# Optimization experiments

Measured on AMD Instinct MI355X. Metric: run time of the kernel, lower is better.

Reference implementation:

```python
import jax, jax.numpy as jnp
import numpy as np

F = 32        # nFilters
OPS = 5       # numOfOps (len(ratio))
CIN = 32      # in_planes of each filter's conv
N, H, W = 16, 128, 128
EPS = 1e-5    # BatchNorm2d default eps
RATIO = [0.3125, 0.3125, 0.1875, 0.125, 0.0625]


def setup_inputs() -> dict:
    key = jax.random.key(0)
    k1, k2 = jax.random.split(key, 2)
    x = jax.random.normal(k1, (N, CIN, H, W), jnp.float32)
    # each filter holds OPS weight variants (one per quantization op); 1 output channel each
    W_all = jax.random.normal(k2, (F, OPS, CIN, 3, 3), jnp.float32) * 0.05
    gamma = jnp.ones((F,), jnp.float32)
    beta = jnp.zeros((F,), jnp.float32)
    # setFiltersRatio: assign op index i to int(ratio[i]*F) consecutive filters
    counts = [int(r * F) for r in RATIO]
    counts[-1] = F - sum(counts[:-1])
    op_idx = jnp.asarray(np.repeat(np.arange(OPS), counts), jnp.int32)  # [F]
    return {"x": x, "W_all": W_all, "gamma": gamma, "beta": beta, "op_idx": op_idx}


def reference(x, W_all, gamma, beta, op_idx):
    # per-filter selection of the active op's conv weight (irregular gather)
    Wsel = W_all[jnp.arange(W_all.shape[0]), op_idx]  # [F, CIN, 3, 3]
    # all per-filter 1-out-channel convs of the same x == one grouped conv to F channels
    out1 = jax.lax.conv_general_dilated(
        x, Wsel, window_strides=(1, 1), padding="SAME",
        dimension_numbers=("NCHW", "OIHW", "NCHW"))  # [N, F, H, W]
    # BatchNorm2d in training mode: batch statistics over (N, H, W) per channel
    mean = out1.mean(axis=(0, 2, 3), keepdims=True)
    var = ((out1 - mean) ** 2).mean(axis=(0, 2, 3), keepdims=True)
    out1 = (out1 - mean) * jax.lax.rsqrt(var + EPS)
    out1 = out1 * gamma[None, :, None, None] + beta[None, :, None, None]
    # op[1] per filter: (quantized) ReLU activation — same math for every op variant
    return jax.nn.relu(out1)
```

## Files before the change

### kernel.cpp

```cpp
#include <hip/hip_runtime.h>

#define NB   16
#define CINC 32
#define HH   128
#define WWD  128
#define FF   32
#define OPSN 5
#define EPSV 1e-5f

#define WS_PARTIAL_FOFF 64
#define WS_WFRAG_BOFF   262400
#define WS_XT_BOFF      280832
#define WS_NEED         (280832 + (size_t)16*130*130*32*2)

typedef __attribute__((ext_vector_type(8))) short bf16x8;
typedef __attribute__((ext_vector_type(4))) float f32x4;
typedef __attribute__((ext_vector_type(4))) unsigned int u32x4;

__device__ __forceinline__ unsigned short f2bf(float f) {
    unsigned u = __builtin_bit_cast(unsigned, f);
    u += 0x7FFFu + ((u >> 16) & 1u);
    return (unsigned short)(u >> 16);
}
__device__ __forceinline__ unsigned pack2(float lo, float hi) {
    return (unsigned)f2bf(lo) | ((unsigned)f2bf(hi) << 16);
}

__global__ __launch_bounds__(256) void transform_kernel(
    const float* __restrict__ x, const float* __restrict__ Wall,
    const int* __restrict__ opidx, unsigned short* __restrict__ xt,
    unsigned short* __restrict__ wfrag)
{
    __shared__ float lds[128 * 35];
    const int bid = blockIdx.x;
    const int tid = threadIdx.x;

    if (bid == NB * 130) {
        for (int idx = tid; idx < 9216; idx += 256) {
            int frag = idx >> 9;
            int lane = (idx >> 3) & 63;
            int j    = idx & 7;
            int s = frag >> 1, m = frag & 1;
            int kh = s / 3, kw = s - 3 * kh;
            int f = m * 16 + (lane & 15);
            int c = ((lane >> 4) << 3) + j;
            float v = Wall[((size_t)(f * OPSN + opidx[f]) * 288) + c * 9 + kh * 3 + kw];
            wfrag[idx] = f2bf(v);
        }
        return;
    }

    const int idx = bid >> 3;
    const int n   = (bid & 7) * 2 + (idx / 130);
    const int hp  = idx % 130;

    unsigned short* rowp = xt + (size_t)(n * 130 + hp) * 130 * 32;
    uint4 zz = make_uint4(0, 0, 0, 0);

    if (hp == 0 || hp == 129) {
        for (int c = tid; c < 520; c += 256) ((uint4*)rowp)[c] = zz;
        return;
    }

    const int h = hp - 1;
    const float* xr = x + ((size_t)n * CINC * HH + h) * WWD;
    const int c  = tid >> 3;
    const int wq = tid & 7;
#pragma unroll
    for (int it = 0; it < 4; ++it) {
        int w4 = wq + it * 8;
        f32x4 v = __builtin_nontemporal_load(
            (const f32x4*)(xr + (size_t)c * (HH * WWD)) + w4);
        int w = w4 * 4;
        lds[(w + 0) * 35 + c] = v.x;
        lds[(w + 1) * 35 + c] = v.y;
        lds[(w + 2) * 35 + c] = v.z;
        lds[(w + 3) * 35 + c] = v.w;
    }
    __syncthreads();
    for (int cc = tid; cc < 512; cc += 256) {
        int p = cc >> 2, k = cc & 3;
        const float* s = &lds[p * 35 + k * 8];
        uint4 o;
        o.x = pack2(s[0], s[1]); o.y = pack2(s[2], s[3]);
        o.z = pack2(s[4], s[5]); o.w = pack2(s[6], s[7]);
        ((uint4*)rowp)[4 + cc] = o;
    }
    if (tid < 4)       ((uint4*)rowp)[tid] = zz;
    else if (tid < 8)  ((uint4*)rowp)[129 * 4 + tid - 4] = zz;
}

#define LOADROW(f0, f1, f2, R)                                                  \
    {                                                                           \
        const unsigned short* rp =                                              \
            xbase + ((size_t)(R) * 130 + w0) * 32 + laneoff;                    \
        f0 = *(const bf16x8*)(rp);                                              \
        f1 = *(const bf16x8*)(rp + 32);                                         \
        f2 = *(const bf16x8*)(rp + 64);                                         \
    }

#define MROW(f0, f1, f2, aA, aB, kh)                                            \
    {                                                                           \
        aA = __builtin_amdgcn_mfma_f32_16x16x32_bf16(wfr[2*((kh)*3+0)],   f0, aA, 0,0,0); \
        aB = __builtin_amdgcn_mfma_f32_16x16x32_bf16(wfr[2*((kh)*3+0)+1], f0, aB, 0,0,0); \
        aA = __builtin_amdgcn_mfma_f32_16x16x32_bf16(wfr[2*((kh)*3+1)],   f1, aA, 0,0,0); \
        aB = __builtin_amdgcn_mfma_f32_16x16x32_bf16(wfr[2*((kh)*3+1)+1], f1, aB, 0,0,0); \
        aA = __builtin_amdgcn_mfma_f32_16x16x32_bf16(wfr[2*((kh)*3+2)],   f2, aA, 0,0,0); \
        aB = __builtin_amdgcn_mfma_f32_16x16x32_bf16(wfr[2*((kh)*3+2)+1], f2, aB, 0,0,0); \
    }

#define CONV_PROLOGUE                                                           \
    bf16x8 wfr[18];                                                             \
    _Pragma("unroll")                                                           \
    for (int i = 0; i < 18; ++i)                                                \
        wfr[i] = *(const bf16x8*)(wfrag + (i * 64 + lane) * 8);                 \
    const unsigned short* xbase = xt + (size_t)n * 130 * 130 * 32;              \
    const int laneoff = l15 * 32 + lhi * 8;                                     \
    f32x4 zz4 = {0.f, 0.f, 0.f, 0.f};                                           \
    f32x4 a0A = zz4, a0B = zz4, a1A = zz4, a1B = zz4;                           \
    f32x4 a2A = zz4, a2B = zz4, a3A = zz4, a3B = zz4;                           \
    bf16x8 c0, c1, c2, n0, n1, n2;                                              \
    LOADROW(c0, c1, c2, h0);                                                    \
    LOADROW(n0, n1, n2, h0 + 1);

#define CONV_BODY(FIN)                                                          \
    MROW(c0, c1, c2, a0A, a0B, 0);                                              \
    LOADROW(c0, c1, c2, h0 + 2);                                                \
    MROW(n0, n1, n2, a0A, a0B, 1);                                              \
    MROW(n0, n1, n2, a1A, a1B, 0);                                              \
    LOADROW(n0, n1, n2, h0 + 3);                                                \
    MROW(c0, c1, c2, a0A, a0B, 2);                                              \
    MROW(c0, c1, c2, a1A, a1B, 1);                                              \
    MROW(c0, c1, c2, a2A, a2B, 0);                                              \
    FIN(a0A, a0B, 0);                                                           \
    LOADROW(c0, c1, c2, h0 + 4);                                                \
    MROW(n0, n1, n2, a1A, a1B, 2);                                              \
    MROW(n0, n1, n2, a2A, a2B, 1);                                              \
    MROW(n0, n1, n2, a3A, a3B, 0);                                              \
    FIN(a1A, a1B, 1);                                                           \
    LOADROW(n0, n1, n2, h0 + 5);                                                \
    MROW(c0, c1, c2, a2A, a2B, 2);                                              \
    MROW(c0, c1, c2, a3A, a3B, 1);                                              \
    FIN(a2A, a2B, 2);                                                           \
    MROW(n0, n1, n2, a3A, a3B, 2);                                              \
    FIN(a3A, a3B, 3);

__global__ __launch_bounds__(256) void conv_stats_kernel(
    const unsigned short* __restrict__ xt,
    const unsigned short* __restrict__ wfrag,
    float* __restrict__ partial)
{
    __shared__ float red[4][64];
    const int bid  = blockIdx.x;
    const int tid  = threadIdx.x;
    const int n    = (bid & 7) * 2 + ((bid >> 3) & 1);
    const int rest = bid >> 4;
    const int h0   = (rest & 31) * 4;
    const int wh   = rest >> 5;
    const int lane = tid & 63;
    const int wv   = tid >> 6;
    const int w0   = wh * 64 + wv * 16;
    const int l15  = lane & 15, lhi = lane >> 4;

    float s8[8], q8[8];
#pragma unroll
    for (int j = 0; j < 8; ++j) { s8[j] = 0.f; q8[j] = 0.f; }

#define FIN_STATS(aA, aB, hh)                                                   \
    {                                                                           \
        _Pragma("unroll")                                                       \
        for (int r = 0; r < 4; ++r) {                                           \
            float v0 = aA[r], v1 = aB[r];                                       \
            s8[r]     += v0;  q8[r]     += v0 * v0;                             \
            s8[4 + r] += v1;  q8[4 + r] += v1 * v1;                             \
        }                                                                       \
    }

    CONV_PROLOGUE
    CONV_BODY(FIN_STATS)
#undef FIN_STATS

#pragma unroll
    for (int m = 1; m < 16; m <<= 1) {
#pragma unroll
        for (int j = 0; j < 8; ++j) {
            s8[j] += __shfl_xor(s8[j], m, 64);
            q8[j] += __shfl_xor(q8[j], m, 64);
        }
    }
    if (l15 == 0) {
#pragma unroll
        for (int j = 0; j < 8; ++j) {
            int f = (j < 4) ? (lhi * 4 + j) : (16 + lhi * 4 + (j - 4));
            red[wv][f]      = s8[j];
            red[wv][32 + f] = q8[j];
        }
    }
    __syncthreads();
    if (tid < 64)
        partial[(size_t)bid * 64 + tid] =
            red[0][tid] + red[1][tid] + red[2][tid] + red[3][tid];
}

__global__ __launch_bounds__(256) void stats2_kernel(
    const float* __restrict__ partial, const float* __restrict__ gamma,
    const float* __restrict__ beta, float* __restrict__ bnp)
{
    __shared__ float rs[256], rq[256];
    const int f = blockIdx.x;
    const int tid = threadIdx.x;
    float s = 0.f, q = 0.f;
#pragma unroll
    for (int k = 0; k < 4; ++k) {
        const float* p = partial + (size_t)(tid * 4 + k) * 64;
        s += p[f];
        q += p[32 + f];
    }
    rs[tid] = s; rq[tid] = q;
    __syncthreads();
    for (int st = 128; st > 0; st >>= 1) {
        if (tid < st) { rs[tid] += rs[tid + st]; rq[tid] += rq[tid + st]; }
        __syncthreads();
    }
    if (tid == 0) {
        float cnt = (float)(NB * HH * WWD);
        float mean = rs[0] / cnt;
        float var  = rq[0] / cnt - mean * mean;
        float sc = gamma[f] * rsqrtf(var + EPSV);
        bnp[f]      = sc;
        bnp[FF + f] = beta[f] - mean * sc;
    }
}

__global__ __launch_bounds__(256) void conv_apply_kernel(
    const unsigned short* __restrict__ xt,
    const unsigned short* __restrict__ wfrag,
    const float* __restrict__ bnp, float* __restrict__ out)
{
    __shared__ float bns[64];
    const int bid  = blockIdx.x;
    const int tid  = threadIdx.x;
    if (tid < 64) bns[tid] = bnp[tid];

    const int n    = (bid & 7) * 2 + ((bid >> 3) & 1);
    const int rest = bid >> 4;
    const int h0   = (rest & 31) * 4;
    const int wh   = rest >> 5;
    const int lane = tid & 63;
    const int wv   = tid >> 6;
    const int w0   = wh * 64 + wv * 16;
    const int l15  = lane & 15, lhi = lane >> 4;

    __syncthreads();
    float sc0[4], sh0[4], sc1[4], sh1[4];
#pragma unroll
    for (int r = 0; r < 4; ++r) {
        int f0 = lhi * 4 + r, f1 = 16 + lhi * 4 + r;
        sc0[r] = bns[f0]; sh0[r] = bns[32 + f0];
        sc1[r] = bns[f1]; sh1[r] = bns[32 + f1];
    }

    float* ob = out + (size_t)(n * FF + lhi * 4) * (HH * WWD) + h0 * WWD + w0 + l15;

#define FIN_APPLY(aA, aB, hh)                                                   \
    {                                                                           \
        _Pragma("unroll")                                                       \
        for (int r = 0; r < 4; ++r) {                                           \
            __builtin_nontemporal_store(                                        \
                fmaxf(fmaf(aA[r], sc0[r], sh0[r]), 0.f),                        \
                ob + (size_t)r * (HH * WWD) + (hh) * WWD);                      \
            __builtin_nontemporal_store(                                        \
                fmaxf(fmaf(aB[r], sc1[r], sh1[r]), 0.f),                        \
                ob + (size_t)r * (HH * WWD) + 16 * (HH * WWD) + (hh) * WWD);    \
        }                                                                       \
    }

    CONV_PROLOGUE
    CONV_BODY(FIN_APPLY)
#undef FIN_APPLY
}

__global__ __launch_bounds__(256) void conv_kernel(
    const float* __restrict__ x, const float* __restrict__ Wall,
    const int* __restrict__ opidx, float* __restrict__ out)
{
    __shared__ float wlds[FF * 289];
    __shared__ float xlds[8 * 3 * 132];
    const int tid = threadIdx.x;
    const int h = blockIdx.x;
    const int n = blockIdx.y;
    for (int i = tid; i < FF * 288; i += 256) {
        int f = i / 288;
        int r = i - f * 288;
        int op = opidx[f];
        wlds[f * 289 + r] = Wall[(f * OPSN + op) * 288 + r];
    }
    const int f = tid & 31;
    const int wg = tid >> 5;
    const int w0 = wg << 4;
    float acc[16];
#pragma unroll
    for (int i = 0; i < 16; ++i) acc[i] = 0.f;
    const float* xn = x + (size_t)n * CINC * HH * WWD;
    for (int cc = 0; cc < 4; ++cc) {
        __syncthreads();
        for (int i = tid; i < 8 * 3 * 132; i += 256) {
            int c8 = i / (3 * 132);
            int rem = i - c8 * (3 * 132);
            int r = rem / 132;
            int wp = rem - r * 132;
            int hin = h + r - 1;
            int win = wp - 1;
            float v = 0.f;
            if ((unsigned)hin < HH && (unsigned)win < WWD)
                v = xn[((cc * 8 + c8) * HH + hin) * WWD + win];
            xlds[i] = v;
        }
        __syncthreads();
#pragma unroll
        for (int c8 = 0; c8 < 8; ++c8) {
            const int c = cc * 8 + c8;
            float wv[9];
#pragma unroll
            for (int k = 0; k < 9; ++k) wv[k] = wlds[f * 289 + c * 9 + k];
#pragma unroll
            for (int kh = 0; kh < 3; ++kh) {
                float xr[20];
                const float4* p = (const float4*)&xlds[(c8 * 3 + kh) * 132 + w0];
#pragma unroll
                for (int j = 0; j < 5; ++j) {
                    float4 v = p[j];
                    xr[j * 4 + 0] = v.x; xr[j * 4 + 1] = v.y;
                    xr[j * 4 + 2] = v.z; xr[j * 4 + 3] = v.w;
                }
#pragma unroll
                for (int kw = 0; kw < 3; ++kw) {
                    float wgt = wv[kh * 3 + kw];
#pragma unroll
                    for (int i = 0; i < 16; ++i)
                        acc[i] = fmaf(xr[i + kw], wgt, acc[i]);
                }
            }
        }
    }
    float* op_ = out + (((size_t)(n * FF + f) * HH + h) * WWD + w0);
#pragma unroll
    for (int j = 0; j < 4; ++j)
        ((float4*)op_)[j] = make_float4(acc[j * 4], acc[j * 4 + 1],
                                        acc[j * 4 + 2], acc[j * 4 + 3]);
}

__global__ __launch_bounds__(256) void stats_kernel(
    const float* __restrict__ out, const float* __restrict__ gamma,
    const float* __restrict__ beta, float* __restrict__ ws)
{
    __shared__ float ssum[256], ssq[256];
    const int f = blockIdx.x;
    const int tid = threadIdx.x;
    float s = 0.f, q = 0.f;
    for (int n = 0; n < NB; ++n) {
        const float4* p = (const float4*)(out + (size_t)(n * FF + f) * HH * WWD);
        for (int i = tid; i < HH * WWD / 4; i += 256) {
            float4 v = p[i];
            s += v.x + v.y + v.z + v.w;
            q += v.x * v.x + v.y * v.y + v.z * v.z + v.w * v.w;
        }
    }
    ssum[tid] = s; ssq[tid] = q;
    __syncthreads();
    for (int st = 128; st > 0; st >>= 1) {
        if (tid < st) { ssum[tid] += ssum[tid + st]; ssq[tid] += ssq[tid + st]; }
        __syncthreads();
    }
    if (tid == 0) {
        float cnt = (float)(NB * HH * WWD);
        float mean = ssum[0] / cnt;
        float var = ssq[0] / cnt - mean * mean;
        float sc = gamma[f] * rsqrtf(var + EPSV);
        ws[f] = sc;
        ws[FF + f] = beta[f] - mean * sc;
    }
}

__global__ __launch_bounds__(256) void apply_kernel(
    float* __restrict__ out, const float* __restrict__ bnp)
{
    const int total4 = NB * FF * HH * WWD / 4;
    for (int i = blockIdx.x * 256 + threadIdx.x; i < total4; i += gridDim.x * 256) {
        int f = (i >> 12) & 31;
        float sc = bnp[f], sh = bnp[FF + f];
        float4 v = ((const float4*)out)[i];
        v.x = fmaxf(fmaf(v.x, sc, sh), 0.f);
        v.y = fmaxf(fmaf(v.y, sc, sh), 0.f);
        v.z = fmaxf(fmaf(v.z, sc, sh), 0.f);
        v.w = fmaxf(fmaf(v.w, sc, sh), 0.f);
        ((float4*)out)[i] = v;
    }
}

extern "C" void kernel_launch(void* const* d_in, const int* in_sizes, int n_in,
                              void* d_out, int out_size, void* d_ws, size_t ws_size,
                              hipStream_t stream) {
    const float* x     = (const float*)d_in[0];
    const float* Wall  = (const float*)d_in[1];
    const float* gamma = (const float*)d_in[2];
    const float* beta  = (const float*)d_in[3];
    const int*   opidx = (const int*)d_in[4];
    float* out = (float*)d_out;
    float* ws  = (float*)d_ws;

    if (ws_size >= WS_NEED) {
        float*          bnp     = ws;
        float*          partial = ws + WS_PARTIAL_FOFF;
        unsigned short* wfrag   = (unsigned short*)((char*)d_ws + WS_WFRAG_BOFF);
        unsigned short* xt      = (unsigned short*)((char*)d_ws + WS_XT_BOFF);

        transform_kernel<<<NB * 130 + 1, 256, 0, stream>>>(x, Wall, opidx, xt, wfrag);
        conv_stats_kernel<<<1024, 256, 0, stream>>>(xt, wfrag, partial);
        stats2_kernel<<<FF, 256, 0, stream>>>(partial, gamma, beta, bnp);
        conv_apply_kernel<<<1024, 256, 0, stream>>>(xt, wfrag, bnp, out);
    } else {
        dim3 gridc(HH, NB);
        conv_kernel<<<gridc, 256, 0, stream>>>(x, Wall, opidx, out);
        stats_kernel<<<FF, 256, 0, stream>>>(out, gamma, beta, ws);
        apply_kernel<<<2048, 256, 0, stream>>>(out, ws);
    }
}
```

Measured before the change: 45.71 us.

## Fuse input transform into stats conv pass via LDS halo tiles

Removes the separate transform kernel. The stats-pass conv now loads fp32 input with halo directly into LDS as packed bf16 and, as it goes, writes its owned region of the padded bf16 copy for the apply pass. Weight fragment preparation moves into each block's LDS for the stats pass and into stats2_kernel for the apply pass. This saves a kernel launch and one global round trip of the transformed input. The price is strided scalar fp32 loads across channels and redundant per-block weight gathering.

```diff
diff --git a/kernel.cpp b/kernel.cpp
--- a/kernel.cpp
+++ b/kernel.cpp
@@ -15,7 +15,6 @@
 
 typedef __attribute__((ext_vector_type(8))) short bf16x8;
 typedef __attribute__((ext_vector_type(4))) float f32x4;
-typedef __attribute__((ext_vector_type(4))) unsigned int u32x4;
 
 __device__ __forceinline__ unsigned short f2bf(float f) {
     unsigned u = __builtin_bit_cast(unsigned, f);
@@ -25,79 +24,6 @@
 __device__ __forceinline__ unsigned pack2(float lo, float hi) {
     return (unsigned)f2bf(lo) | ((unsigned)f2bf(hi) << 16);
 }
-
-__global__ __launch_bounds__(256) void transform_kernel(
-    const float* __restrict__ x, const float* __restrict__ Wall,
-    const int* __restrict__ opidx, unsigned short* __restrict__ xt,
-    unsigned short* __restrict__ wfrag)
-{
-    __shared__ float lds[128 * 35];
-    const int bid = blockIdx.x;
-    const int tid = threadIdx.x;
-
-    if (bid == NB * 130) {
-        for (int idx = tid; idx < 9216; idx += 256) {
-            int frag = idx >> 9;
-            int lane = (idx >> 3) & 63;
-            int j    = idx & 7;
-            int s = frag >> 1, m = frag & 1;
-            int kh = s / 3, kw = s - 3 * kh;
-            int f = m * 16 + (lane & 15);
-            int c = ((lane >> 4) << 3) + j;
-            float v = Wall[((size_t)(f * OPSN + opidx[f]) * 288) + c * 9 + kh * 3 + kw];
-            wfrag[idx] = f2bf(v);
-        }
-        return;
-    }
-
-    const int idx = bid >> 3;
-    const int n   = (bid & 7) * 2 + (idx / 130);
-    const int hp  = idx % 130;
-
-    unsigned short* rowp = xt + (size_t)(n * 130 + hp) * 130 * 32;
-    uint4 zz = make_uint4(0, 0, 0, 0);
-
-    if (hp == 0 || hp == 129) {
-        for (int c = tid; c < 520; c += 256) ((uint4*)rowp)[c] = zz;
-        return;
-    }
-
-    const int h = hp - 1;
-    const float* xr = x + ((size_t)n * CINC * HH + h) * WWD;
-    const int c  = tid >> 3;
-    const int wq = tid & 7;
-#pragma unroll
-    for (int it = 0; it < 4; ++it) {
-        int w4 = wq + it * 8;
-        f32x4 v = __builtin_nontemporal_load(
-            (const f32x4*)(xr + (size_t)c * (HH * WWD)) + w4);
-        int w = w4 * 4;
-        lds[(w + 0) * 35 + c] = v.x;
-        lds[(w + 1) * 35 + c] = v.y;
-        lds[(w + 2) * 35 + c] = v.z;
-        lds[(w + 3) * 35 + c] = v.w;
-    }
-    __syncthreads();
-    for (int cc = tid; cc < 512; cc += 256) {
-        int p = cc >> 2, k = cc & 3;
-        const float* s = &lds[p * 35 + k * 8];
-        uint4 o;
-        o.x = pack2(s[0], s[1]); o.y = pack2(s[2], s[3]);
-        o.z = pack2(s[4], s[5]); o.w = pack2(s[6], s[7]);
-        ((uint4*)rowp)[4 + cc] = o;
-    }
-    if (tid < 4)       ((uint4*)rowp)[tid] = zz;
-    else if (tid < 8)  ((uint4*)rowp)[129 * 4 + tid - 4] = zz;
-}
-
-#define LOADROW(f0, f1, f2, R)                                                  \
-    {                                                                           \
-        const unsigned short* rp =                                              \
-            xbase + ((size_t)(R) * 130 + w0) * 32 + laneoff;                    \
-        f0 = *(const bf16x8*)(rp);                                              \
-        f1 = *(const bf16x8*)(rp + 32);                                         \
-        f2 = *(const bf16x8*)(rp + 64);                                         \
-    }
 
 #define MROW(f0, f1, f2, aA, aB, kh)                                            \
     {                                                                           \
@@ -109,48 +35,15 @@
         aB = __builtin_amdgcn_mfma_f32_16x16x32_bf16(wfr[2*((kh)*3+2)+1], f2, aB, 0,0,0); \
     }
 
-#define CONV_PROLOGUE                                                           \
-    bf16x8 wfr[18];                                                             \
-    _Pragma("unroll")                                                           \
-    for (int i = 0; i < 18; ++i)                                                \
-        wfr[i] = *(const bf16x8*)(wfrag + (i * 64 + lane) * 8);                 \
-    const unsigned short* xbase = xt + (size_t)n * 130 * 130 * 32;              \
-    const int laneoff = l15 * 32 + lhi * 8;                                     \
-    f32x4 zz4 = {0.f, 0.f, 0.f, 0.f};                                           \
-    f32x4 a0A = zz4, a0B = zz4, a1A = zz4, a1B = zz4;                           \
-    f32x4 a2A = zz4, a2B = zz4, a3A = zz4, a3B = zz4;                           \
-    bf16x8 c0, c1, c2, n0, n1, n2;                                              \
-    LOADROW(c0, c1, c2, h0);                                                    \
-    LOADROW(n0, n1, n2, h0 + 1);
-
-#define CONV_BODY(FIN)                                                          \
-    MROW(c0, c1, c2, a0A, a0B, 0);                                              \
-    LOADROW(c0, c1, c2, h0 + 2);                                                \
-    MROW(n0, n1, n2, a0A, a0B, 1);                                              \
-    MROW(n0, n1, n2, a1A, a1B, 0);                                              \
-    LOADROW(n0, n1, n2, h0 + 3);                                                \
-    MROW(c0, c1, c2, a0A, a0B, 2);                                              \
-    MROW(c0, c1, c2, a1A, a1B, 1);                                              \
-    MROW(c0, c1, c2, a2A, a2B, 0);                                              \
-    FIN(a0A, a0B, 0);                                                           \
-    LOADROW(c0, c1, c2, h0 + 4);                                                \
-    MROW(n0, n1, n2, a1A, a1B, 2);                                              \
-    MROW(n0, n1, n2, a2A, a2B, 1);                                              \
-    MROW(n0, n1, n2, a3A, a3B, 0);                                              \
-    FIN(a1A, a1B, 1);                                                           \
-    LOADROW(n0, n1, n2, h0 + 5);                                                \
-    MROW(c0, c1, c2, a2A, a2B, 2);                                              \
-    MROW(c0, c1, c2, a3A, a3B, 1);                                              \
-    FIN(a2A, a2B, 2);                                                           \
-    MROW(n0, n1, n2, a3A, a3B, 2);                                              \
-    FIN(a3A, a3B, 3);
-
-__global__ __launch_bounds__(256) void conv_stats_kernel(
-    const unsigned short* __restrict__ xt,
-    const unsigned short* __restrict__ wfrag,
+__global__ __launch_bounds__(256) void fused_stats_kernel(
+    const float* __restrict__ x, const float* __restrict__ Wall,
+    const int* __restrict__ opidx, unsigned short* __restrict__ xt,
     float* __restrict__ partial)
 {
+    __shared__ unsigned short wtile[18 * 64 * 8];
+    __shared__ unsigned short XL[6 * 66 * 32];
     __shared__ float red[4][64];
+
     const int bid  = blockIdx.x;
     const int tid  = threadIdx.x;
     const int n    = (bid & 7) * 2 + ((bid >> 3) & 1);
@@ -159,14 +52,77 @@
     const int wh   = rest >> 5;
     const int lane = tid & 63;
     const int wv   = tid >> 6;
-    const int w0   = wh * 64 + wv * 16;
     const int l15  = lane & 15, lhi = lane >> 4;
+    const int w0   = wh * 64;
+
+    for (int idx = tid; idx < 9216; idx += 256) {
+        int frag = idx >> 9;
+        int ln   = (idx >> 3) & 63;
+        int j    = idx & 7;
+        int s = frag >> 1, m = frag & 1;
+        int kh = s / 3, kw = s - 3 * kh;
+        int f = m * 16 + (ln & 15);
+        int c = ((ln >> 4) << 3) + j;
+        wtile[idx] = f2bf(Wall[(size_t)(f * OPSN + opidx[f]) * 288 + c * 9 + kh * 3 + kw]);
+    }
+
+    const float* xn = x + (size_t)n * (CINC * HH * WWD);
+    for (int pos = tid; pos < 396; pos += 256) {
+        int row = pos / 66;
+        int wpl = pos - row * 66;
+        int h_in = h0 + row - 1;
+        int w_in = w0 + wpl - 1;
+        unsigned pk[16];
+        if ((unsigned)h_in < HH && (unsigned)w_in < WWD) {
+            const float* xp = xn + (size_t)h_in * WWD + w_in;
+#pragma unroll
+            for (int cp = 0; cp < 16; ++cp) {
+                float v0 = xp[(size_t)(2 * cp) * (HH * WWD)];
+                float v1 = xp[(size_t)(2 * cp + 1) * (HH * WWD)];
+                pk[cp] = pack2(v0, v1);
+            }
+        } else {
+#pragma unroll
+            for (int cp = 0; cp < 16; ++cp) pk[cp] = 0u;
+        }
+        uint4* dst = (uint4*)&XL[(row * 66 + wpl) * 32];
+        dst[0] = make_uint4(pk[0],  pk[1],  pk[2],  pk[3]);
+        dst[1] = make_uint4(pk[4],  pk[5],  pk[6],  pk[7]);
+        dst[2] = make_uint4(pk[8],  pk[9],  pk[10], pk[11]);
+        dst[3] = make_uint4(pk[12], pk[13], pk[14], pk[15]);
+
+        bool ownr = (row >= 1 && row <= 4) || (row == 0 && h0 == 0) || (row == 5 && h0 == 124);
+        bool ownw = (wpl >= 1 && wpl <= 64) || (wpl == 0 && w0 == 0) || (wpl == 65 && w0 == 64);
+        if (ownr && ownw) {
+            int hp = h0 + row;
+            int wp = w0 + wpl;
+            uint4* gp = (uint4*)(xt + ((size_t)(n * 130 + hp) * 130 + wp) * 32);
+            gp[0] = make_uint4(pk[0],  pk[1],  pk[2],  pk[3]);
+            gp[1] = make_uint4(pk[4],  pk[5],  pk[6],  pk[7]);
+            gp[2] = make_uint4(pk[8],  pk[9],  pk[10], pk[11]);
+            gp[3] = make_uint4(pk[12], pk[13], pk[14], pk[15]);
+        }
+    }
+    __syncthreads();
+
+    bf16x8 wfr[18];
+#pragma unroll
+    for (int i = 0; i < 18; ++i)
+        wfr[i] = *(const bf16x8*)(&wtile[(i * 64 + lane) * 8]);
+
+#define LROW(f0, f1, f2, RL)                                                    \
+    {                                                                           \
+        const unsigned short* rp = &XL[((RL) * 66 + wv * 16 + l15) * 32 + lhi * 8]; \
+        f0 = *(const bf16x8*)(rp);                                              \
+        f1 = *(const bf16x8*)(rp + 32);                                         \
+        f2 = *(const bf16x8*)(rp + 64);                                         \
+    }
 
     float s8[8], q8[8];
 #pragma unroll
     for (int j = 0; j < 8; ++j) { s8[j] = 0.f; q8[j] = 0.f; }
 
-#define FIN_STATS(aA, aB, hh)                                                   \
+#define FINS(aA, aB)                                                            \
     {                                                                           \
         _Pragma("unroll")                                                       \
         for (int r = 0; r < 4; ++r) {                                           \
@@ -176,9 +132,34 @@
         }                                                                       \
     }
 
-    CONV_PROLOGUE
-    CONV_BODY(FIN_STATS)
-#undef FIN_STATS
+    f32x4 zz4 = {0.f, 0.f, 0.f, 0.f};
+    f32x4 a0A = zz4, a0B = zz4, a1A = zz4, a1B = zz4;
+    f32x4 a2A = zz4, a2B = zz4, a3A = zz4, a3B = zz4;
+    bf16x8 c0, c1, c2, n0, n1, n2;
+    LROW(c0, c1, c2, 0);
+    LROW(n0, n1, n2, 1);
+    MROW(c0, c1, c2, a0A, a0B, 0);
+    LROW(c0, c1, c2, 2);
+    MROW(n0, n1, n2, a0A, a0B, 1);
+    MROW(n0, n1, n2, a1A, a1B, 0);
+    LROW(n0, n1, n2, 3);
+    MROW(c0, c1, c2, a0A, a0B, 2);
+    MROW(c0, c1, c2, a1A, a1B, 1);
+    MROW(c0, c1, c2, a2A, a2B, 0);
+    FINS(a0A, a0B);
+    LROW(c0, c1, c2, 4);
+    MROW(n0, n1, n2, a1A, a1B, 2);
+    MROW(n0, n1, n2, a2A, a2B, 1);
+    MROW(n0, n1, n2, a3A, a3B, 0);
+    FINS(a1A, a1B);
+    LROW(n0, n1, n2, 5);
+    MROW(c0, c1, c2, a2A, a2B, 2);
+    MROW(c0, c1, c2, a3A, a3B, 1);
+    FINS(a2A, a2B);
+    MROW(n0, n1, n2, a3A, a3B, 2);
+    FINS(a3A, a3B);
+#undef FINS
+#undef LROW
 
 #pragma unroll
     for (int m = 1; m < 16; m <<= 1) {
@@ -204,11 +185,27 @@
 
 __global__ __launch_bounds__(256) void stats2_kernel(
     const float* __restrict__ partial, const float* __restrict__ gamma,
-    const float* __restrict__ beta, float* __restrict__ bnp)
+    const float* __restrict__ beta, float* __restrict__ bnp,
+    const float* __restrict__ Wall, const int* __restrict__ opidx,
+    unsigned short* __restrict__ wfrag)
 {
     __shared__ float rs[256], rq[256];
     const int f = blockIdx.x;
     const int tid = threadIdx.x;
+
+    if (f == 0) {
+        for (int idx = tid; idx < 9216; idx += 256) {
+            int frag = idx >> 9;
+            int ln   = (idx >> 3) & 63;
+            int j    = idx & 7;
+            int s = frag >> 1, m = frag & 1;
+            int kh = s / 3, kw = s - 3 * kh;
+            int ff = m * 16 + (ln & 15);
+            int c  = ((ln >> 4) << 3) + j;
+            wfrag[idx] = f2bf(Wall[(size_t)(ff * OPSN + opidx[ff]) * 288 + c * 9 + kh * 3 + kw]);
+        }
+    }
+
     float s = 0.f, q = 0.f;
 #pragma unroll
     for (int k = 0; k < 4; ++k) {
@@ -231,6 +228,15 @@
         bnp[FF + f] = beta[f] - mean * sc;
     }
 }
+
+#define LOADROW(f0, f1, f2, R)                                                  \
+    {                                                                           \
+        const unsigned short* rp =                                              \
+            xbase + ((size_t)(R) * 130 + w0) * 32 + laneoff;                    \
+        f0 = *(const bf16x8*)(rp);                                              \
+        f1 = *(const bf16x8*)(rp + 32);                                         \
+        f2 = *(const bf16x8*)(rp + 64);                                         \
+    }
 
 __global__ __launch_bounds__(256) void conv_apply_kernel(
     const unsigned short* __restrict__ xt,
@@ -251,6 +257,14 @@
     const int w0   = wh * 64 + wv * 16;
     const int l15  = lane & 15, lhi = lane >> 4;
 
+    bf16x8 wfr[18];
+#pragma unroll
+    for (int i = 0; i < 18; ++i)
+        wfr[i] = *(const bf16x8*)(wfrag + (i * 64 + lane) * 8);
+
+    const unsigned short* xbase = xt + (size_t)n * 130 * 130 * 32;
+    const int laneoff = l15 * 32 + lhi * 8;
+
     __syncthreads();
     float sc0[4], sh0[4], sc1[4], sh1[4];
 #pragma unroll
@@ -259,6 +273,13 @@
         sc0[r] = bns[f0]; sh0[r] = bns[32 + f0];
         sc1[r] = bns[f1]; sh1[r] = bns[32 + f1];
     }
+
+    f32x4 zz4 = {0.f, 0.f, 0.f, 0.f};
+    f32x4 a0A = zz4, a0B = zz4, a1A = zz4, a1B = zz4;
+    f32x4 a2A = zz4, a2B = zz4, a3A = zz4, a3B = zz4;
+    bf16x8 c0, c1, c2, n0, n1, n2;
+    LOADROW(c0, c1, c2, h0);
+    LOADROW(n0, n1, n2, h0 + 1);
 
     float* ob = out + (size_t)(n * FF + lhi * 4) * (HH * WWD) + h0 * WWD + w0 + l15;
 
@@ -275,8 +296,26 @@
         }                                                                       \
     }
 
-    CONV_PROLOGUE
-    CONV_BODY(FIN_APPLY)
+    MROW(c0, c1, c2, a0A, a0B, 0);
+    LOADROW(c0, c1, c2, h0 + 2);
+    MROW(n0, n1, n2, a0A, a0B, 1);
+    MROW(n0, n1, n2, a1A, a1B, 0);
+    LOADROW(n0, n1, n2, h0 + 3);
+    MROW(c0, c1, c2, a0A, a0B, 2);
+    MROW(c0, c1, c2, a1A, a1B, 1);
+    MROW(c0, c1, c2, a2A, a2B, 0);
+    FIN_APPLY(a0A, a0B, 0);
+    LOADROW(c0, c1, c2, h0 + 4);
+    MROW(n0, n1, n2, a1A, a1B, 2);
+    MROW(n0, n1, n2, a2A, a2B, 1);
+    MROW(n0, n1, n2, a3A, a3B, 0);
+    FIN_APPLY(a1A, a1B, 1);
+    LOADROW(n0, n1, n2, h0 + 5);
+    MROW(c0, c1, c2, a2A, a2B, 2);
+    MROW(c0, c1, c2, a3A, a3B, 1);
+    FIN_APPLY(a2A, a2B, 2);
+    MROW(n0, n1, n2, a3A, a3B, 2);
+    FIN_APPLY(a3A, a3B, 3);
 #undef FIN_APPLY
 }
 
@@ -415,9 +454,9 @@
         unsigned short* wfrag   = (unsigned short*)((char*)d_ws + WS_WFRAG_BOFF);
         unsigned short* xt      = (unsigned short*)((char*)d_ws + WS_XT_BOFF);
 
-        transform_kernel<<<NB * 130 + 1, 256, 0, stream>>>(x, Wall, opidx, xt, wfrag);
-        conv_stats_kernel<<<1024, 256, 0, stream>>>(xt, wfrag, partial);
-        stats2_kernel<<<FF, 256, 0, stream>>>(partial, gamma, beta, bnp);
+        fused_stats_kernel<<<1024, 256, 0, stream>>>(x, Wall, opidx, xt, partial);
+        stats2_kernel<<<FF, 256, 0, stream>>>(partial, gamma, beta, bnp,
+                                              Wall, opidx, wfrag);
         conv_apply_kernel<<<1024, 256, 0, stream>>>(xt, wfrag, bnp, out);
     } else {
         dim3 gridc(HH, NB);
```

After: 56.02 us. +22.5%, slower.

## Fuse BN stats finalization into apply kernel via per-batch atomic accumulators

Applied to the files above, without the earlier changes.

Removes the separate stats2 kernel launch. Each conv_stats block now atomically adds its per-channel sum and sum-of-squares into a 16x64 accumulator indexed by batch element. The accumulator is zeroed by the weight-prep block of the transform kernel. Every conv_apply block reduces the 16 slices and computes scale and shift itself. The x load also switches from a nontemporal load to a plain float4 load. The atomics and the redundant per-block finalization add a little work in exchange for one fewer launch and dependency gap, and atomic ordering makes the sums nondeterministic.

```diff
diff --git a/kernel.cpp b/kernel.cpp
--- a/kernel.cpp
+++ b/kernel.cpp
@@ -8,14 +8,12 @@
 #define OPSN 5
 #define EPSV 1e-5f
 
-#define WS_PARTIAL_FOFF 64
 #define WS_WFRAG_BOFF   262400
 #define WS_XT_BOFF      280832
 #define WS_NEED         (280832 + (size_t)16*130*130*32*2)
 
 typedef __attribute__((ext_vector_type(8))) short bf16x8;
 typedef __attribute__((ext_vector_type(4))) float f32x4;
-typedef __attribute__((ext_vector_type(4))) unsigned int u32x4;
 
 __device__ __forceinline__ unsigned short f2bf(float f) {
     unsigned u = __builtin_bit_cast(unsigned, f);
@@ -29,13 +27,14 @@
 __global__ __launch_bounds__(256) void transform_kernel(
     const float* __restrict__ x, const float* __restrict__ Wall,
     const int* __restrict__ opidx, unsigned short* __restrict__ xt,
-    unsigned short* __restrict__ wfrag)
+    unsigned short* __restrict__ wfrag, float* __restrict__ acc)
 {
     __shared__ float lds[128 * 35];
     const int bid = blockIdx.x;
     const int tid = threadIdx.x;
 
     if (bid == NB * 130) {
+        for (int i = tid; i < 1024; i += 256) acc[i] = 0.f;
         for (int idx = tid; idx < 9216; idx += 256) {
             int frag = idx >> 9;
             int lane = (idx >> 3) & 63;
@@ -69,8 +68,7 @@
 #pragma unroll
     for (int it = 0; it < 4; ++it) {
         int w4 = wq + it * 8;
-        f32x4 v = __builtin_nontemporal_load(
-            (const f32x4*)(xr + (size_t)c * (HH * WWD)) + w4);
+        float4 v = ((const float4*)(xr + (size_t)c * (HH * WWD)))[w4];
         int w = w4 * 4;
         lds[(w + 0) * 35 + c] = v.x;
         lds[(w + 1) * 35 + c] = v.y;
@@ -148,7 +146,7 @@
 __global__ __launch_bounds__(256) void conv_stats_kernel(
     const unsigned short* __restrict__ xt,
     const unsigned short* __restrict__ wfrag,
-    float* __restrict__ partial)
+    float* __restrict__ acc)
 {
     __shared__ float red[4][64];
     const int bid  = blockIdx.x;
@@ -197,50 +195,39 @@
         }
     }
     __syncthreads();
-    if (tid < 64)
-        partial[(size_t)bid * 64 + tid] =
-            red[0][tid] + red[1][tid] + red[2][tid] + red[3][tid];
-}
-
-__global__ __launch_bounds__(256) void stats2_kernel(
-    const float* __restrict__ partial, const float* __restrict__ gamma,
-    const float* __restrict__ beta, float* __restrict__ bnp)
-{
-    __shared__ float rs[256], rq[256];
-    const int f = blockIdx.x;
-    const int tid = threadIdx.x;
-    float s = 0.f, q = 0.f;
-#pragma unroll
-    for (int k = 0; k < 4; ++k) {
-        const float* p = partial + (size_t)(tid * 4 + k) * 64;
-        s += p[f];
-        q += p[32 + f];
-    }
-    rs[tid] = s; rq[tid] = q;
-    __syncthreads();
-    for (int st = 128; st > 0; st >>= 1) {
-        if (tid < st) { rs[tid] += rs[tid + st]; rq[tid] += rq[tid + st]; }
-        __syncthreads();
-    }
-    if (tid == 0) {
-        float cnt = (float)(NB * HH * WWD);
-        float mean = rs[0] / cnt;
-        float var  = rq[0] / cnt - mean * mean;
-        float sc = gamma[f] * rsqrtf(var + EPSV);
-        bnp[f]      = sc;
-        bnp[FF + f] = beta[f] - mean * sc;
+    if (tid < 64) {
+        float v = red[0][tid] + red[1][tid] + red[2][tid] + red[3][tid];
+        atomicAdd(&acc[n * 64 + tid], v);
     }
 }
 
 __global__ __launch_bounds__(256) void conv_apply_kernel(
     const unsigned short* __restrict__ xt,
     const unsigned short* __restrict__ wfrag,
-    const float* __restrict__ bnp, float* __restrict__ out)
-{
+    const float* __restrict__ acc,
+    const float* __restrict__ gamma, const float* __restrict__ beta,
+    float* __restrict__ out)
+{
+    __shared__ float tot[64];
     __shared__ float bns[64];
     const int bid  = blockIdx.x;
     const int tid  = threadIdx.x;
-    if (tid < 64) bns[tid] = bnp[tid];
+
+    if (tid < 64) {
+        float s = 0.f;
+#pragma unroll
+        for (int k = 0; k < 16; ++k) s += acc[k * 64 + tid];
+        tot[tid] = s;
+    }
+    __syncthreads();
+    if (tid < 32) {
+        float cnt  = (float)(NB * HH * WWD);
+        float mean = tot[tid] / cnt;
+        float var  = tot[32 + tid] / cnt - mean * mean;
+        float sc   = gamma[tid] * rsqrtf(var + EPSV);
+        bns[tid]      = sc;
+        bns[32 + tid] = beta[tid] - mean * sc;
+    }
 
     const int n    = (bid & 7) * 2 + ((bid >> 3) & 1);
     const int rest = bid >> 4;
@@ -410,15 +397,13 @@
     float* ws  = (float*)d_ws;
 
     if (ws_size >= WS_NEED) {
-        float*          bnp     = ws;
-        float*          partial = ws + WS_PARTIAL_FOFF;
-        unsigned short* wfrag   = (unsigned short*)((char*)d_ws + WS_WFRAG_BOFF);
-        unsigned short* xt      = (unsigned short*)((char*)d_ws + WS_XT_BOFF);
-
-        transform_kernel<<<NB * 130 + 1, 256, 0, stream>>>(x, Wall, opidx, xt, wfrag);
-        conv_stats_kernel<<<1024, 256, 0, stream>>>(xt, wfrag, partial);
-        stats2_kernel<<<FF, 256, 0, stream>>>(partial, gamma, beta, bnp);
-        conv_apply_kernel<<<1024, 256, 0, stream>>>(xt, wfrag, bnp, out);
+        float*          acc   = ws;
+        unsigned short* wfrag = (unsigned short*)((char*)d_ws + WS_WFRAG_BOFF);
+        unsigned short* xt    = (unsigned short*)((char*)d_ws + WS_XT_BOFF);
+
+        transform_kernel<<<NB * 130 + 1, 256, 0, stream>>>(x, Wall, opidx, xt, wfrag, acc);
+        conv_stats_kernel<<<1024, 256, 0, stream>>>(xt, wfrag, acc);
+        conv_apply_kernel<<<1024, 256, 0, stream>>>(xt, wfrag, acc, gamma, beta, out);
     } else {
         dim3 gridc(HH, NB);
         conv_kernel<<<gridc, 256, 0, stream>>>(x, Wall, opidx, out);
```

Measured after the change: 43.32 us. 1.06x faster.
